# Performance work log

Hardware: AMD Instinct MI355X
Metric: run time of the kernel (lower is better)

## Reference

```python
import jax, jax.numpy as jnp
import numpy as np

N = 100000      # nodes
E = 1600000     # edges (avg degree 16)
D = 64          # in_dim == hidden_dim
L = 4           # layer_gin
G = 128         # graphs in batch
BN_EPS = 1e-5


def setup_inputs() -> dict:
    key = jax.random.key(0)
    ks = jax.random.split(key, 9)
    x = jax.random.normal(ks[0], (N, D), dtype=jnp.float32)
    edge_index = jax.random.randint(ks[1], (2, E), 0, N, dtype=jnp.int32)
    batch = jnp.sort(jax.random.randint(ks[2], (N,), 0, G, dtype=jnp.int32))
    s = 0.05
    W1 = jax.random.normal(ks[3], (L, D, D), dtype=jnp.float32) * s
    b1 = jax.random.normal(ks[4], (L, D), dtype=jnp.float32) * s
    gamma = jnp.ones((L, D), dtype=jnp.float32)
    beta = jnp.zeros((L, D), dtype=jnp.float32)
    W2 = jax.random.normal(ks[5], (L, D, D), dtype=jnp.float32) * s
    b2 = jax.random.normal(ks[6], (L, D), dtype=jnp.float32) * s
    return dict(x=x, edge_index=edge_index, batch=batch,
                W1=W1, b1=b1, gamma=gamma, beta=beta, W2=W2, b2=b2)


def reference(x, edge_index, batch, W1, b1, gamma, beta, W2, b2):
    n = x.shape[0]
    src, dst = edge_index[0], edge_index[1]  # flow source_to_target
    # in-degree for mean aggregation (clamped to avoid div-by-zero)
    deg = jax.ops.segment_sum(jnp.ones(src.shape, x.dtype), dst, num_segments=n)
    inv_deg = 1.0 / jnp.maximum(deg, 1.0)
    # graph sizes for global mean pool
    gcnt = jax.ops.segment_sum(jnp.ones((n,), x.dtype), batch, num_segments=G)
    inv_gcnt = 1.0 / jnp.maximum(gcnt, 1.0)

    h = x
    node_pool = jnp.zeros((n, W2.shape[-1]), x.dtype)
    g_pool = jnp.zeros((G, W2.shape[-1]), x.dtype)
    for l in range(L):  # small fixed layer count
        # scatter-mean neighbor aggregation: [E,D] gather -> segment_sum
        agg = jax.ops.segment_sum(h[src], dst, num_segments=n) * inv_deg[:, None]
        z = (h + agg) @ W1[l] + b1[l]          # eps=0: (1+eps)*x + mean_j x_j
        mu = z.mean(axis=0)
        var = z.var(axis=0)                     # biased, as torch BatchNorm1d
        z = (z - mu) * jax.lax.rsqrt(var + BN_EPS) * gamma[l] + beta[l]
        h = jax.nn.relu(z) @ W2[l] + b2[l]
        node_pool = node_pool + h
        g_pool = g_pool + jax.ops.segment_sum(h, batch, num_segments=G) * inv_gcnt[:, None]
    return node_pool, g_pool
```

## Files before the change

kernel.cpp:

```cpp
#include <hip/hip_runtime.h>

#define N_NODES 100000
#define N_EDGES 1600000
#define DIM 64
#define NLAYER 4
#define NGRAPH 128
#define BN_EPS 1e-5f
#define NSHARD 16
#define AGG_CHUNK 16

typedef unsigned short ushort_t;
typedef unsigned int uint_t;
typedef __attribute__((ext_vector_type(8))) short short8;
typedef __attribute__((ext_vector_type(4))) float f32x4;

__device__ __forceinline__ ushort_t f2bf(float f) {
    uint_t u = __float_as_uint(f);
    uint_t r = (u + 0x7FFFu + ((u >> 16) & 1u)) >> 16;
    return (ushort_t)r;
}
__device__ __forceinline__ float bf2f(ushort_t u) {
    return __uint_as_float((uint_t)u << 16);
}
__device__ __forceinline__ void bf8_to_f32(const uint4 v, float f[8]) {
    f[0] = __uint_as_float(v.x << 16);
    f[1] = __uint_as_float(v.x & 0xFFFF0000u);
    f[2] = __uint_as_float(v.y << 16);
    f[3] = __uint_as_float(v.y & 0xFFFF0000u);
    f[4] = __uint_as_float(v.z << 16);
    f[5] = __uint_as_float(v.z & 0xFFFF0000u);
    f[6] = __uint_as_float(v.w << 16);
    f[7] = __uint_as_float(v.w & 0xFFFF0000u);
}


__global__ void k_hist(const int* __restrict__ ei, int* __restrict__ cntS,
                       int* __restrict__ rank) {
    int e = blockIdx.x * blockDim.x + threadIdx.x;
    if (e < N_EDGES) {
        int d = ei[N_EDGES + e];
        int s = blockIdx.x & (NSHARD - 1);
        rank[e] = atomicAdd(&cntS[s * N_NODES + d], 1);
    }
}

__global__ void k_sumsh(int* __restrict__ cntS, int* __restrict__ cnt) {
    int i = blockIdx.x * blockDim.x + threadIdx.x;
    if (i < N_NODES) {
        int run = 0;
#pragma unroll
        for (int s = 0; s < NSHARD; s++) {
            int c = cntS[s * N_NODES + i];
            cntS[s * N_NODES + i] = run;
            run += c;
        }
        cnt[i] = run;
    }
}

__global__ void k_scan1(const int* __restrict__ cnt, int* __restrict__ exc,
                        int* __restrict__ bsums) {
    __shared__ int s[256];
    int i = blockIdx.x * 256 + threadIdx.x;
    int v = (i < N_NODES) ? cnt[i] : 0;
    s[threadIdx.x] = v;
    __syncthreads();
    for (int off = 1; off < 256; off <<= 1) {
        int t = (threadIdx.x >= off) ? s[threadIdx.x - off] : 0;
        __syncthreads();
        s[threadIdx.x] += t;
        __syncthreads();
    }
    if (i < N_NODES) exc[i] = s[threadIdx.x] - v;
    if (threadIdx.x == 255) bsums[blockIdx.x] = s[255];
}

__global__ void k_scan2(const int* __restrict__ bsums, int* __restrict__ boffs, int nb) {
    __shared__ int s[512];
    int v = ((int)threadIdx.x < nb) ? bsums[threadIdx.x] : 0;
    s[threadIdx.x] = v;
    __syncthreads();
    for (int off = 1; off < 512; off <<= 1) {
        int t = (threadIdx.x >= off) ? s[threadIdx.x - off] : 0;
        __syncthreads();
        s[threadIdx.x] += t;
        __syncthreads();
    }
    if ((int)threadIdx.x < nb) boffs[threadIdx.x] = s[threadIdx.x] - v;
}

__global__ void k_scan3(int* __restrict__ exc, const int* __restrict__ boffs) {
    int i = blockIdx.x * 256 + threadIdx.x;
    if (i < N_NODES) exc[i] += boffs[blockIdx.x];
}

__global__ void k_fill(const int* __restrict__ ei, const int* __restrict__ rowptr,
                       const int* __restrict__ cntS, const int* __restrict__ rank,
                       int* __restrict__ csr) {
    int e = blockIdx.x * blockDim.x + threadIdx.x;
    if (e < N_EDGES) {
        int d = ei[N_EDGES + e];
        int s = blockIdx.x & (NSHARD - 1);
        csr[rowptr[d] + cntS[s * N_NODES + d] + rank[e]] = ei[e];
    }
}

__global__ void k_prep(const int* __restrict__ cnt, const int* __restrict__ batch,
                       float* __restrict__ invdeg, float* __restrict__ invg) {
    int i = blockIdx.x * blockDim.x + threadIdx.x;
    if (i < N_NODES) invdeg[i] = 1.0f / (float)max(cnt[i], 1);
    if (i < NGRAPH) {
        int key = i, lo = 0, hi = N_NODES;
        while (lo < hi) { int m = (lo + hi) >> 1; if (batch[m] < key) lo = m + 1; else hi = m; }
        int a = lo;
        key = i + 1; lo = 0; hi = N_NODES;
        while (lo < hi) { int m = (lo + hi) >> 1; if (batch[m] < key) lo = m + 1; else hi = m; }
        invg[i] = 1.0f / (float)max(lo - a, 1);
    }
}

__global__ void k_xcast(const float* __restrict__ x, ushort_t* __restrict__ xh) {
    int i = blockIdx.x * blockDim.x + threadIdx.x;
    if (i < N_NODES * 16) {
        const float4 v = ((const float4*)x)[i];
        ushort4 u;
        u.x = f2bf(v.x); u.y = f2bf(v.y); u.z = f2bf(v.z); u.w = f2bf(v.w);
        ((ushort4*)xh)[i] = u;
    }
}

__device__ __forceinline__ void grp8b(const ushort_t* __restrict__ h,
                                      const int* __restrict__ cp,
                                      int e, int deg, int q, int r,
                                      float acc[8]) {
    const int last = deg - 1;
    const int e0 = e + q;
    int i0 = cp[min(e0, last)];
    float m0 = (e0 < deg) ? 1.f : 0.f;
    const uint4 v = *(const uint4*)(h + (size_t)i0 * 64 + r * 8);
    float f[8];
    bf8_to_f32(v, f);
#pragma unroll
    for (int j = 0; j < 8; j++) acc[j] = fmaf(f[j], m0, acc[j]);
}


__global__ __launch_bounds__(256, 4)
void k_passA(const ushort_t* __restrict__ h, const float* __restrict__ W1,
             const float* __restrict__ b1,
             const int* __restrict__ rowptr, const int* __restrict__ cnt,
             const int* __restrict__ csr, const float* __restrict__ invdeg,
             float* __restrict__ z, float* __restrict__ colsum,
             float* __restrict__ colsumsq) {
    __shared__ ushort_t wfrag[512 * 8];
    __shared__ uint_t smt[4][16 * 36];
    __shared__ float red[128];

    const int w = threadIdx.x >> 6;
    const int lane = threadIdx.x & 63;
    const int q = lane >> 3;
    const int r = lane & 7;
    const int wid = __builtin_amdgcn_readfirstlane((blockIdx.x << 2) | w);
    const bool active = wid < (N_NODES / AGG_CHUNK);
    const int n0 = (active ? wid : 0) * AGG_CHUNK;

    for (int s = threadIdx.x; s < 512; s += 256) {
        const int hh = s >> 8, c = (s >> 6) & 3, L = s & 63;
        const int kb = hh * 32 + ((L >> 4) * 8);
        const int out = c * 16 + (L & 15);
        uint_t* dst = (uint_t*)&wfrag[s * 8];
#pragma unroll
        for (int j2 = 0; j2 < 4; j2++) {
            const float lo = W1[(kb + 2 * j2) * 64 + out];
            const float hi = W1[(kb + 2 * j2 + 1) * 64 + out];
            dst[j2] = (uint_t)f2bf(lo) | ((uint_t)f2bf(hi) << 16);
        }
    }
    if (threadIdx.x < 128) red[threadIdx.x] = 0.f;
    __syncthreads();

    if (active) {
        for (int pp = 0; pp < AGG_CHUNK; pp += 2) {
            const int n = n0 + pp;
            const int sa = rowptr[n],     da = cnt[n];
            const int sb = rowptr[n + 1], db = cnt[n + 1];
            const float idga = invdeg[n], idgb = invdeg[n + 1];
            const int* __restrict__ ca = csr + sa;
            const int* __restrict__ cb = csr + sb;

            float aa[8] = {0,0,0,0,0,0,0,0};
            float ab[8] = {0,0,0,0,0,0,0,0};
            const int mm = min(da, db);
            int e = 0;
            for (; e < mm; e += 8) {
                grp8b(h, ca, e, da, q, r, aa);
                grp8b(h, cb, e, db, q, r, ab);
            }
            for (; e < da; e += 8) grp8b(h, ca, e, da, q, r, aa);
            for (; e < db; e += 8) grp8b(h, cb, e, db, q, r, ab);

#pragma unroll
            for (int j = 0; j < 8; j++) {
                aa[j] += __shfl_xor(aa[j], 8, 64);
                aa[j] += __shfl_xor(aa[j], 16, 64);
                aa[j] += __shfl_xor(aa[j], 32, 64);
                ab[j] += __shfl_xor(ab[j], 8, 64);
                ab[j] += __shfl_xor(ab[j], 16, 64);
                ab[j] += __shfl_xor(ab[j], 32, 64);
            }

            const uint4 sva = *(const uint4*)(h + (size_t)n * 64 + r * 8);
            const uint4 svb = *(const uint4*)(h + (size_t)(n + 1) * 64 + r * 8);
            float sa8[8], sb8[8];
            bf8_to_f32(sva, sa8);
            bf8_to_f32(svb, sb8);
            float ta[8], tb[8];
#pragma unroll
            for (int j = 0; j < 8; j++) {
                ta[j] = fmaf(aa[j], idga, sa8[j]);
                tb[j] = fmaf(ab[j], idgb, sb8[j]);
            }

            if (q < 2) {
                const int row = pp + q;
                uint_t* dst = &smt[w][row * 36 + r * 4];
#pragma unroll
                for (int j2 = 0; j2 < 4; j2++) {
                    const float lo = q ? tb[2 * j2]     : ta[2 * j2];
                    const float hi = q ? tb[2 * j2 + 1] : ta[2 * j2 + 1];
                    dst[j2] = (uint_t)f2bf(lo) | ((uint_t)f2bf(hi) << 16);
                }
            }
        }
    }
    __syncthreads();

    const int m = lane & 15;
    const int quad = lane >> 4;
    const short8 a0 = *(const short8*)&smt[w][m * 36 + quad * 4];
    const short8 a1 = *(const short8*)&smt[w][m * 36 + 16 + quad * 4];

    float lsum[4], lsq[4];
#pragma unroll
    for (int c = 0; c < 4; c++) {
        const short8 b0 = *(const short8*)&wfrag[(size_t)(c * 64 + lane) * 8];
        const short8 b1f = *(const short8*)&wfrag[(size_t)((4 + c) * 64 + lane) * 8];
        f32x4 D = {0.f, 0.f, 0.f, 0.f};
        D = __builtin_amdgcn_mfma_f32_16x16x32_bf16(a0, b0, D, 0, 0, 0);
        D = __builtin_amdgcn_mfma_f32_16x16x32_bf16(a1, b1f, D, 0, 0, 0);
        const float bv = b1[c * 16 + m];
        float s = 0.f, sq = 0.f;
#pragma unroll
        for (int reg = 0; reg < 4; reg++) {
            const float zv = D[reg] + bv;
            if (active) {
                const int node = n0 + quad * 4 + reg;
                __builtin_nontemporal_store(zv, &z[(size_t)node * 64 + c * 16 + m]);
            }
            s += zv;
            sq += zv * zv;
        }
        lsum[c] = s;
        lsq[c] = sq;
    }

    if (active) {
#pragma unroll
        for (int c = 0; c < 4; c++) {
            float s = lsum[c], sq = lsq[c];
            s += __shfl_xor(s, 16, 64);
            s += __shfl_xor(s, 32, 64);
            sq += __shfl_xor(sq, 16, 64);
            sq += __shfl_xor(sq, 32, 64);
            if (quad == 0) {
                atomicAdd(&red[c * 16 + m], s);
                atomicAdd(&red[64 + c * 16 + m], sq);
            }
        }
    }
    __syncthreads();
    if (threadIdx.x < 64) {
        atomicAdd(&colsum[threadIdx.x], red[threadIdx.x]);
        atomicAdd(&colsumsq[threadIdx.x], red[64 + threadIdx.x]);
    }
}


__global__ __launch_bounds__(256, 4)
void k_passB(const float* __restrict__ z, const float* __restrict__ W2,
             const float* __restrict__ b2, const float* __restrict__ colsum,
             const float* __restrict__ colsumsq, const float* __restrict__ gamma,
             const float* __restrict__ beta, ushort_t* __restrict__ hout) {
    __shared__ ushort_t wfrag[512 * 8];
    __shared__ float sscale[64], sshift[64];
    __shared__ float ltile[4][16 * 68];

    const int w = threadIdx.x >> 6;
    const int lane = threadIdx.x & 63;
    const int wid = __builtin_amdgcn_readfirstlane((blockIdx.x << 2) | w);
    const bool active = wid < (N_NODES / 16);
    const int n0 = (active ? wid : 0) * 16;

    for (int s = threadIdx.x; s < 512; s += 256) {
        const int hh = s >> 8, c = (s >> 6) & 3, L = s & 63;
        const int kb = hh * 32 + ((L >> 4) * 8);
        const int out = c * 16 + (L & 15);
        uint_t* dst = (uint_t*)&wfrag[s * 8];
#pragma unroll
        for (int j2 = 0; j2 < 4; j2++) {
            const float lo = W2[(kb + 2 * j2) * 64 + out];
            const float hi = W2[(kb + 2 * j2 + 1) * 64 + out];
            dst[j2] = (uint_t)f2bf(lo) | ((uint_t)f2bf(hi) << 16);
        }
    }
    if (threadIdx.x < 64) {
        const float invn = 1.0f / (float)N_NODES;
        const float mu = colsum[threadIdx.x] * invn;
        const float var = colsumsq[threadIdx.x] * invn - mu * mu;
        const float sc = gamma[threadIdx.x] * rsqrtf(var + BN_EPS);
        sscale[threadIdx.x] = sc;
        sshift[threadIdx.x] = beta[threadIdx.x] - mu * sc;
    }
    __syncthreads();

    const int m = lane & 15;
    const int quad = lane >> 4;

    const float* zp = z + (size_t)(n0 + m) * 64;
    const f32x4 za = __builtin_nontemporal_load((const f32x4*)(zp + quad * 8));
    const f32x4 zb = __builtin_nontemporal_load((const f32x4*)(zp + quad * 8 + 4));
    const f32x4 zc = __builtin_nontemporal_load((const f32x4*)(zp + 32 + quad * 8));
    const f32x4 zd = __builtin_nontemporal_load((const f32x4*)(zp + 32 + quad * 8 + 4));
    const f32x4 c0 = *(const f32x4*)&sscale[quad * 8];
    const f32x4 c1 = *(const f32x4*)&sscale[quad * 8 + 4];
    const f32x4 c2 = *(const f32x4*)&sscale[32 + quad * 8];
    const f32x4 c3 = *(const f32x4*)&sscale[32 + quad * 8 + 4];
    const f32x4 h0 = *(const f32x4*)&sshift[quad * 8];
    const f32x4 h1v = *(const f32x4*)&sshift[quad * 8 + 4];
    const f32x4 h2v = *(const f32x4*)&sshift[32 + quad * 8];
    const f32x4 h3v = *(const f32x4*)&sshift[32 + quad * 8 + 4];

    float r0[8], r1[8];
#pragma unroll
    for (int j = 0; j < 4; j++) {
        r0[j]     = fmaxf(fmaf(za[j], c0[j], h0[j]), 0.f);
        r0[4 + j] = fmaxf(fmaf(zb[j], c1[j], h1v[j]), 0.f);
        r1[j]     = fmaxf(fmaf(zc[j], c2[j], h2v[j]), 0.f);
        r1[4 + j] = fmaxf(fmaf(zd[j], c3[j], h3v[j]), 0.f);
    }
    union { uint_t u[4]; short8 v; } pa0, pa1;
#pragma unroll
    for (int j2 = 0; j2 < 4; j2++) {
        pa0.u[j2] = (uint_t)f2bf(r0[2 * j2]) | ((uint_t)f2bf(r0[2 * j2 + 1]) << 16);
        pa1.u[j2] = (uint_t)f2bf(r1[2 * j2]) | ((uint_t)f2bf(r1[2 * j2 + 1]) << 16);
    }
    const short8 a0 = pa0.v;
    const short8 a1 = pa1.v;

#pragma unroll
    for (int c = 0; c < 4; c++) {
        const short8 b0 = *(const short8*)&wfrag[(size_t)(c * 64 + lane) * 8];
        const short8 b1f = *(const short8*)&wfrag[(size_t)((4 + c) * 64 + lane) * 8];
        f32x4 D = {0.f, 0.f, 0.f, 0.f};
        D = __builtin_amdgcn_mfma_f32_16x16x32_bf16(a0, b0, D, 0, 0, 0);
        D = __builtin_amdgcn_mfma_f32_16x16x32_bf16(a1, b1f, D, 0, 0, 0);
        const float bv = b2[c * 16 + m];
#pragma unroll
        for (int reg = 0; reg < 4; reg++)
            ltile[w][(quad * 4 + reg) * 68 + c * 16 + m] = D[reg] + bv;
    }

    if (active) {
#pragma unroll
        for (int n = 0; n < 16; n++) {
            const float hv = ltile[w][n * 68 + lane];
            hout[(size_t)(n0 + n) * 64 + lane] = f2bf(hv);
        }
    }
}


#define POOL_CHUNK 64

__global__ void k_pool(const ushort_t* __restrict__ h1, const ushort_t* __restrict__ h2,
                       const ushort_t* __restrict__ h3, const ushort_t* __restrict__ h4,
                       const int* __restrict__ batch, float* __restrict__ node_pool,
                       float* __restrict__ gacc) {
    const int lane = threadIdx.x & 63;
    const int wid = (blockIdx.x << 2) | (threadIdx.x >> 6);
    const int n0 = wid * POOL_CHUNK;
    if (n0 >= N_NODES) return;
    const int n1 = min(N_NODES, n0 + POOL_CHUNK);
    int curg = -1;
    float ga = 0.f;
    for (int n = n0; n < n1; n++) {
        const size_t off = (size_t)n * 64 + lane;
        const float v = bf2f(h1[off]) + bf2f(h2[off]) + bf2f(h3[off]) + bf2f(h4[off]);
        __builtin_nontemporal_store(v, &node_pool[off]);
        const int g = batch[n];
        if (g != curg) {
            if (curg >= 0) atomicAdd(&gacc[curg * 64 + lane], ga);
            ga = 0.f;
            curg = g;
        }
        ga += v;
    }
    if (curg >= 0) atomicAdd(&gacc[curg * 64 + lane], ga);
}

__global__ void k_gfinal(const float* __restrict__ gacc, const float* __restrict__ invg,
                         float* __restrict__ gout) {
    int i = blockIdx.x * blockDim.x + threadIdx.x;
    if (i < NGRAPH * 64) gout[i] = gacc[i] * invg[i >> 6];
}


extern "C" void kernel_launch(void* const* d_in, const int* in_sizes, int n_in,
                              void* d_out, int out_size, void* d_ws, size_t ws_size,
                              hipStream_t stream) {
    (void)in_sizes; (void)n_in; (void)out_size; (void)ws_size;
    const float* x     = (const float*)d_in[0];
    const int*   ei    = (const int*)d_in[1];
    const int*   batch = (const int*)d_in[2];
    const float* W1    = (const float*)d_in[3];
    const float* b1    = (const float*)d_in[4];
    const float* gamma = (const float*)d_in[5];
    const float* beta  = (const float*)d_in[6];
    const float* W2    = (const float*)d_in[7];
    const float* b2    = (const float*)d_in[8];
    float* out = (float*)d_out;

    size_t o = 0;
    size_t o_cntS    = o; o += (size_t)NSHARD * N_NODES;
    size_t o_colsum  = o; o += (size_t)NLAYER * 64;
    size_t o_colsq   = o; o += (size_t)NLAYER * 64;
    size_t o_gacc    = o; o += (size_t)NGRAPH * 64;
    size_t zero_elems = o;
    size_t o_cnt     = o; o += N_NODES;
    size_t o_rowptr  = o; o += N_NODES;
    size_t o_bsums   = o; o += 512;
    size_t o_boffs   = o; o += 512;
    size_t o_invdeg  = o; o += N_NODES;
    size_t o_invg    = o; o += NGRAPH;
    size_t o_rank    = o; o += N_EDGES;
    size_t o_csr     = o; o += N_EDGES;
    size_t o_bufA    = o; o += (size_t)N_NODES * 64;
    size_t o_h1      = o; o += (size_t)N_NODES * 32;
    size_t o_h2      = o; o += (size_t)N_NODES * 32;
    size_t o_h3      = o; o += (size_t)N_NODES * 32;
    size_t o_xh      = o; o += (size_t)N_NODES * 32;

    int*   wsi = (int*)d_ws;
    float* wsf = (float*)d_ws;
    int*      cntS   = wsi + o_cntS;
    float*    colsum = wsf + o_colsum;
    float*    colsq  = wsf + o_colsq;
    float*    gacc   = wsf + o_gacc;
    int*      cnt    = wsi + o_cnt;
    int*      rowptr = wsi + o_rowptr;
    int*      bsums  = wsi + o_bsums;
    int*      boffs  = wsi + o_boffs;
    float*    invdeg = wsf + o_invdeg;
    float*    invg   = wsf + o_invg;
    int*      rank   = wsi + o_rank;
    int*      csr    = wsi + o_csr;
    float*    bufA   = wsf + o_bufA;
    ushort_t* hb0    = (ushort_t*)(wsi + o_h1);
    ushort_t* hb1    = (ushort_t*)(wsi + o_h2);
    ushort_t* hb2    = (ushort_t*)(wsi + o_h3);
    ushort_t* xh     = (ushort_t*)(wsi + o_xh);

    hipMemsetAsync(d_ws, 0, zero_elems * 4, stream);

    const int eb = (N_EDGES + 255) / 256;
    const int nb = (N_NODES + 255) / 256;

    k_hist<<<eb, 256, 0, stream>>>(ei, cntS, rank);
    k_xcast<<<(N_NODES * 16 + 255) / 256, 256, 0, stream>>>(x, xh);
    k_sumsh<<<nb, 256, 0, stream>>>(cntS, cnt);
    k_scan1<<<nb, 256, 0, stream>>>(cnt, rowptr, bsums);
    k_scan2<<<1, 512, 0, stream>>>(bsums, boffs, nb);
    k_scan3<<<nb, 256, 0, stream>>>(rowptr, boffs);
    k_prep<<<nb, 256, 0, stream>>>(cnt, batch, invdeg, invg);
    k_fill<<<eb, 256, 0, stream>>>(ei, rowptr, cntS, rank, csr);

    const ushort_t* hin[NLAYER]  = {xh,  hb0, hb1, hb2};
    ushort_t*       hoz[NLAYER]  = {hb0, hb1, hb2, xh};

    const int gridA = (N_NODES / AGG_CHUNK + 3) / 4;
    for (int l = 0; l < NLAYER; l++) {
        k_passA<<<gridA, 256, 0, stream>>>(hin[l], W1 + l * 4096, b1 + l * 64,
                                           rowptr, cnt, csr, invdeg,
                                           bufA, colsum + l * 64, colsq + l * 64);
        k_passB<<<gridA, 256, 0, stream>>>(bufA, W2 + l * 4096, b2 + l * 64,
                                           colsum + l * 64, colsq + l * 64,
                                           gamma + l * 64, beta + l * 64, hoz[l]);
    }
    const int gridP = (N_NODES + POOL_CHUNK * 4 - 1) / (POOL_CHUNK * 4);
    k_pool<<<gridP, 256, 0, stream>>>(hb0, hb1, hb2, xh, batch, out, gacc);
    k_gfinal<<<32, 256, 0, stream>>>(gacc, invg, out + (size_t)N_NODES * 64);
}
```

Before: 571.7 us.

## Split feature gather into quarter-column passes with quartered bf16 layout

Stores node features in a column-quartered bf16 layout (4 slabs of 16 columns), so each aggregation pass gathers only a 3.2 MB slab that can stay cache-resident. Aggregation is split into a separate k_gq kernel launched four times per layer, and the GEMM reads its input from global memory. The CSR build drops the sharded histogram in favour of a single atomic counter per node and pads rows to multiples of 4. The cost is extra launches, an extra write and read of the aggregated tensor, a second layout write in passB, and more atomic contention in the histogram.

```diff
diff --git a/kernel.cpp b/kernel.cpp
--- a/kernel.cpp
+++ b/kernel.cpp
@@ -6,11 +6,12 @@
 #define NLAYER 4
 #define NGRAPH 128
 #define BN_EPS 1e-5f
-#define NSHARD 16
 #define AGG_CHUNK 16
+#define NCHUNK (N_NODES / AGG_CHUNK)
 
 typedef unsigned short ushort_t;
 typedef unsigned int uint_t;
+typedef unsigned long long ull_t;
 typedef __attribute__((ext_vector_type(8))) short short8;
 typedef __attribute__((ext_vector_type(4))) float f32x4;
 
@@ -22,39 +23,20 @@
 __device__ __forceinline__ float bf2f(ushort_t u) {
     return __uint_as_float((uint_t)u << 16);
 }
-__device__ __forceinline__ void bf8_to_f32(const uint4 v, float f[8]) {
+__device__ __forceinline__ void bf4_to_f32(const uint2 v, float f[4]) {
     f[0] = __uint_as_float(v.x << 16);
     f[1] = __uint_as_float(v.x & 0xFFFF0000u);
     f[2] = __uint_as_float(v.y << 16);
     f[3] = __uint_as_float(v.y & 0xFFFF0000u);
-    f[4] = __uint_as_float(v.z << 16);
-    f[5] = __uint_as_float(v.z & 0xFFFF0000u);
-    f[6] = __uint_as_float(v.w << 16);
-    f[7] = __uint_as_float(v.w & 0xFFFF0000u);
-}
-
-
-__global__ void k_hist(const int* __restrict__ ei, int* __restrict__ cntS,
+}
+
+
+__global__ void k_hist(const int* __restrict__ ei, int* __restrict__ cnt,
                        int* __restrict__ rank) {
     int e = blockIdx.x * blockDim.x + threadIdx.x;
     if (e < N_EDGES) {
         int d = ei[N_EDGES + e];
-        int s = blockIdx.x & (NSHARD - 1);
-        rank[e] = atomicAdd(&cntS[s * N_NODES + d], 1);
-    }
-}
-
-__global__ void k_sumsh(int* __restrict__ cntS, int* __restrict__ cnt) {
-    int i = blockIdx.x * blockDim.x + threadIdx.x;
-    if (i < N_NODES) {
-        int run = 0;
-#pragma unroll
-        for (int s = 0; s < NSHARD; s++) {
-            int c = cntS[s * N_NODES + i];
-            cntS[s * N_NODES + i] = run;
-            run += c;
-        }
-        cnt[i] = run;
+        rank[e] = atomicAdd(&cnt[d], 1);
     }
 }
 
@@ -62,7 +44,7 @@
                         int* __restrict__ bsums) {
     __shared__ int s[256];
     int i = blockIdx.x * 256 + threadIdx.x;
-    int v = (i < N_NODES) ? cnt[i] : 0;
+    int v = (i < N_NODES) ? ((cnt[i] + 3) & ~3) : 0;
     s[threadIdx.x] = v;
     __syncthreads();
     for (int off = 1; off < 256; off <<= 1) {
@@ -94,14 +76,12 @@
     if (i < N_NODES) exc[i] += boffs[blockIdx.x];
 }
 
-__global__ void k_fill(const int* __restrict__ ei, const int* __restrict__ rowptr,
-                       const int* __restrict__ cntS, const int* __restrict__ rank,
-                       int* __restrict__ csr) {
+__global__ void k_fill(const int* __restrict__ ei, const int* __restrict__ rowptr4,
+                       const int* __restrict__ rank, int* __restrict__ csr) {
     int e = blockIdx.x * blockDim.x + threadIdx.x;
     if (e < N_EDGES) {
         int d = ei[N_EDGES + e];
-        int s = blockIdx.x & (NSHARD - 1);
-        csr[rowptr[d] + cntS[s * N_NODES + d] + rank[e]] = ei[e];
+        csr[rowptr4[d] + rank[e]] = ei[e];
     }
 }
 
@@ -119,49 +99,90 @@
     }
 }
 
-__global__ void k_xcast(const float* __restrict__ x, ushort_t* __restrict__ xh) {
+__global__ void k_xcastq(const float* __restrict__ x, ushort_t* __restrict__ xq) {
     int i = blockIdx.x * blockDim.x + threadIdx.x;
-    if (i < N_NODES * 16) {
-        const float4 v = ((const float4*)x)[i];
-        ushort4 u;
-        u.x = f2bf(v.x); u.y = f2bf(v.y); u.z = f2bf(v.z); u.w = f2bf(v.w);
-        ((ushort4*)xh)[i] = u;
-    }
-}
-
-__device__ __forceinline__ void grp8b(const ushort_t* __restrict__ h,
-                                      const int* __restrict__ cp,
-                                      int e, int deg, int q, int r,
-                                      float acc[8]) {
-    const int last = deg - 1;
-    const int e0 = e + q;
-    int i0 = cp[min(e0, last)];
-    float m0 = (e0 < deg) ? 1.f : 0.f;
-    const uint4 v = *(const uint4*)(h + (size_t)i0 * 64 + r * 8);
-    float f[8];
-    bf8_to_f32(v, f);
-#pragma unroll
-    for (int j = 0; j < 8; j++) acc[j] = fmaf(f[j], m0, acc[j]);
+    if (i < N_NODES * 32) {
+        const int n = i >> 5, p = i & 31;
+        const float lo = x[(size_t)n * 64 + 2 * p];
+        const float hi = x[(size_t)n * 64 + 2 * p + 1];
+        const uint_t d = (uint_t)f2bf(lo) | ((uint_t)f2bf(hi) << 16);
+        const int q = p >> 3, ci = p & 7;
+        ((uint_t*)xq)[((size_t)q * N_NODES + n) * 8 + ci] = d;
+    }
+}
+
+
+__global__ __launch_bounds__(256, 8)
+void k_gq(const ushort_t* __restrict__ hq, const int* __restrict__ rowptr4,
+          const int* __restrict__ cnt, const int* __restrict__ csr,
+          const float* __restrict__ invdeg, ushort_t* __restrict__ tq, int qtr) {
+    const int lane = threadIdx.x & 63;
+    const int s = lane >> 2;
+    const int c4 = lane & 3;
+    const int wid = (blockIdx.x << 2) | (threadIdx.x >> 6);
+    if (wid >= NCHUNK) return;
+    const int n = wid * AGG_CHUNK + s;
+
+    const size_t qoff = (size_t)qtr * N_NODES * 16;
+    const ushort_t* __restrict__ hs = hq + qoff;
+    ushort_t* __restrict__ ts = (ushort_t*)tq + qoff;
+
+    const int* __restrict__ cp = csr + rowptr4[n];
+    const int deg = cnt[n];
+    int dmax = deg;
+    dmax = max(dmax, __shfl_xor(dmax, 4, 64));
+    dmax = max(dmax, __shfl_xor(dmax, 8, 64));
+    dmax = max(dmax, __shfl_xor(dmax, 16, 64));
+    dmax = max(dmax, __shfl_xor(dmax, 32, 64));
+
+    float acc[4] = {0.f, 0.f, 0.f, 0.f};
+    for (int e = 0; e < dmax; e += 4) {
+        const int i0 = __builtin_nontemporal_load(&cp[e]);
+        const int i1 = __builtin_nontemporal_load(&cp[e + 1]);
+        const int i2 = __builtin_nontemporal_load(&cp[e + 2]);
+        const int i3 = __builtin_nontemporal_load(&cp[e + 3]);
+        const int ia[4] = {i0, i1, i2, i3};
+#pragma unroll
+        for (int k = 0; k < 4; k++) {
+            if (e + k < deg) {
+                const uint2 v = *(const uint2*)(hs + (size_t)(uint_t)ia[k] * 16 + (c4 << 2));
+                float f[4];
+                bf4_to_f32(v, f);
+                acc[0] += f[0];
+                acc[1] += f[1];
+                acc[2] += f[2];
+                acc[3] += f[3];
+            }
+        }
+    }
+
+    const float idg = invdeg[n];
+    const uint2 sv = *(const uint2*)(hs + (size_t)n * 16 + (c4 << 2));
+    float sf[4];
+    bf4_to_f32(sv, sf);
+    const float t0 = fmaf(acc[0], idg, sf[0]);
+    const float t1 = fmaf(acc[1], idg, sf[1]);
+    const float t2 = fmaf(acc[2], idg, sf[2]);
+    const float t3 = fmaf(acc[3], idg, sf[3]);
+    const uint_t d0 = (uint_t)f2bf(t0) | ((uint_t)f2bf(t1) << 16);
+    const uint_t d1 = (uint_t)f2bf(t2) | ((uint_t)f2bf(t3) << 16);
+    uint_t* dst = (uint_t*)(ts + (size_t)n * 16) + (c4 << 1);
+    __builtin_nontemporal_store(d0, dst);
+    __builtin_nontemporal_store(d1, dst + 1);
 }
 
 
 __global__ __launch_bounds__(256, 4)
-void k_passA(const ushort_t* __restrict__ h, const float* __restrict__ W1,
-             const float* __restrict__ b1,
-             const int* __restrict__ rowptr, const int* __restrict__ cnt,
-             const int* __restrict__ csr, const float* __restrict__ invdeg,
-             float* __restrict__ z, float* __restrict__ colsum,
-             float* __restrict__ colsumsq) {
+void k_mmA(const ushort_t* __restrict__ t, const float* __restrict__ W1,
+           const float* __restrict__ b1, float* __restrict__ z,
+           float* __restrict__ colsum, float* __restrict__ colsumsq) {
     __shared__ ushort_t wfrag[512 * 8];
-    __shared__ uint_t smt[4][16 * 36];
     __shared__ float red[128];
 
     const int w = threadIdx.x >> 6;
     const int lane = threadIdx.x & 63;
-    const int q = lane >> 3;
-    const int r = lane & 7;
     const int wid = __builtin_amdgcn_readfirstlane((blockIdx.x << 2) | w);
-    const bool active = wid < (N_NODES / AGG_CHUNK);
+    const bool active = wid < NCHUNK;
     const int n0 = (active ? wid : 0) * AGG_CHUNK;
 
     for (int s = threadIdx.x; s < 512; s += 256) {
@@ -179,66 +200,13 @@
     if (threadIdx.x < 128) red[threadIdx.x] = 0.f;
     __syncthreads();
 
-    if (active) {
-        for (int pp = 0; pp < AGG_CHUNK; pp += 2) {
-            const int n = n0 + pp;
-            const int sa = rowptr[n],     da = cnt[n];
-            const int sb = rowptr[n + 1], db = cnt[n + 1];
-            const float idga = invdeg[n], idgb = invdeg[n + 1];
-            const int* __restrict__ ca = csr + sa;
-            const int* __restrict__ cb = csr + sb;
-
-            float aa[8] = {0,0,0,0,0,0,0,0};
-            float ab[8] = {0,0,0,0,0,0,0,0};
-            const int mm = min(da, db);
-            int e = 0;
-            for (; e < mm; e += 8) {
-                grp8b(h, ca, e, da, q, r, aa);
-                grp8b(h, cb, e, db, q, r, ab);
-            }
-            for (; e < da; e += 8) grp8b(h, ca, e, da, q, r, aa);
-            for (; e < db; e += 8) grp8b(h, cb, e, db, q, r, ab);
-
-#pragma unroll
-            for (int j = 0; j < 8; j++) {
-                aa[j] += __shfl_xor(aa[j], 8, 64);
-                aa[j] += __shfl_xor(aa[j], 16, 64);
-                aa[j] += __shfl_xor(aa[j], 32, 64);
-                ab[j] += __shfl_xor(ab[j], 8, 64);
-                ab[j] += __shfl_xor(ab[j], 16, 64);
-                ab[j] += __shfl_xor(ab[j], 32, 64);
-            }
-
-            const uint4 sva = *(const uint4*)(h + (size_t)n * 64 + r * 8);
-            const uint4 svb = *(const uint4*)(h + (size_t)(n + 1) * 64 + r * 8);
-            float sa8[8], sb8[8];
-            bf8_to_f32(sva, sa8);
-            bf8_to_f32(svb, sb8);
-            float ta[8], tb[8];
-#pragma unroll
-            for (int j = 0; j < 8; j++) {
-                ta[j] = fmaf(aa[j], idga, sa8[j]);
-                tb[j] = fmaf(ab[j], idgb, sb8[j]);
-            }
-
-            if (q < 2) {
-                const int row = pp + q;
-                uint_t* dst = &smt[w][row * 36 + r * 4];
-#pragma unroll
-                for (int j2 = 0; j2 < 4; j2++) {
-                    const float lo = q ? tb[2 * j2]     : ta[2 * j2];
-                    const float hi = q ? tb[2 * j2 + 1] : ta[2 * j2 + 1];
-                    dst[j2] = (uint_t)f2bf(lo) | ((uint_t)f2bf(hi) << 16);
-                }
-            }
-        }
-    }
-    __syncthreads();
-
     const int m = lane & 15;
     const int quad = lane >> 4;
-    const short8 a0 = *(const short8*)&smt[w][m * 36 + quad * 4];
-    const short8 a1 = *(const short8*)&smt[w][m * 36 + 16 + quad * 4];
+    const int node = n0 + m;
+    const short8 a0 = *(const short8*)(t +
+        ((size_t)((quad >> 1) * N_NODES) + node) * 16 + ((quad & 1) << 3));
+    const short8 a1 = *(const short8*)(t +
+        ((size_t)(((quad >> 1) + 2) * N_NODES) + node) * 16 + ((quad & 1) << 3));
 
     float lsum[4], lsq[4];
 #pragma unroll
@@ -254,8 +222,8 @@
         for (int reg = 0; reg < 4; reg++) {
             const float zv = D[reg] + bv;
             if (active) {
-                const int node = n0 + quad * 4 + reg;
-                __builtin_nontemporal_store(zv, &z[(size_t)node * 64 + c * 16 + m]);
+                const int nd = n0 + quad * 4 + reg;
+                __builtin_nontemporal_store(zv, &z[(size_t)nd * 64 + c * 16 + m]);
             }
             s += zv;
             sq += zv * zv;
@@ -290,7 +258,8 @@
 void k_passB(const float* __restrict__ z, const float* __restrict__ W2,
              const float* __restrict__ b2, const float* __restrict__ colsum,
              const float* __restrict__ colsumsq, const float* __restrict__ gamma,
-             const float* __restrict__ beta, ushort_t* __restrict__ hout) {
+             const float* __restrict__ beta, ushort_t* __restrict__ hout,
+             ushort_t* __restrict__ houtq) {
     __shared__ ushort_t wfrag[512 * 8];
     __shared__ float sscale[64], sshift[64];
     __shared__ float ltile[4][16 * 68];
@@ -298,8 +267,8 @@
     const int w = threadIdx.x >> 6;
     const int lane = threadIdx.x & 63;
     const int wid = __builtin_amdgcn_readfirstlane((blockIdx.x << 2) | w);
-    const bool active = wid < (N_NODES / 16);
-    const int n0 = (active ? wid : 0) * 16;
+    const bool active = wid < NCHUNK;
+    const int n0 = (active ? wid : 0) * AGG_CHUNK;
 
     for (int s = threadIdx.x; s < 512; s += 256) {
         const int hh = s >> 8, c = (s >> 6) & 3, L = s & 63;
@@ -371,10 +340,14 @@
     }
 
     if (active) {
+        const int qs = lane >> 4, ci = lane & 15;
 #pragma unroll
         for (int n = 0; n < 16; n++) {
             const float hv = ltile[w][n * 68 + lane];
-            hout[(size_t)(n0 + n) * 64 + lane] = f2bf(hv);
+            const ushort_t b = f2bf(hv);
+            hout[(size_t)(n0 + n) * 64 + lane] = b;
+            if (houtq)
+                houtq[((size_t)qs * N_NODES + (n0 + n)) * 16 + ci] = b;
         }
     }
 }
@@ -431,32 +404,33 @@
     float* out = (float*)d_out;
 
     size_t o = 0;
-    size_t o_cntS    = o; o += (size_t)NSHARD * N_NODES;
+    size_t o_cnt     = o; o += N_NODES;
     size_t o_colsum  = o; o += (size_t)NLAYER * 64;
     size_t o_colsq   = o; o += (size_t)NLAYER * 64;
     size_t o_gacc    = o; o += (size_t)NGRAPH * 64;
     size_t zero_elems = o;
-    size_t o_cnt     = o; o += N_NODES;
     size_t o_rowptr  = o; o += N_NODES;
     size_t o_bsums   = o; o += 512;
     size_t o_boffs   = o; o += 512;
     size_t o_invdeg  = o; o += N_NODES;
     size_t o_invg    = o; o += NGRAPH;
     size_t o_rank    = o; o += N_EDGES;
-    size_t o_csr     = o; o += N_EDGES;
-    size_t o_bufA    = o; o += (size_t)N_NODES * 64;
+    size_t o_csr     = o; o += N_EDGES + 3 * N_NODES + 64;
+    size_t o_z       = o; o += (size_t)N_NODES * 64;
+    size_t o_t       = o; o += (size_t)N_NODES * 32;
+    size_t o_sA      = o; o += (size_t)N_NODES * 32;
+    size_t o_sB      = o; o += (size_t)N_NODES * 32;
+    size_t o_h0      = o; o += (size_t)N_NODES * 32;
     size_t o_h1      = o; o += (size_t)N_NODES * 32;
     size_t o_h2      = o; o += (size_t)N_NODES * 32;
     size_t o_h3      = o; o += (size_t)N_NODES * 32;
-    size_t o_xh      = o; o += (size_t)N_NODES * 32;
 
     int*   wsi = (int*)d_ws;
     float* wsf = (float*)d_ws;
-    int*      cntS   = wsi + o_cntS;
+    int*      cnt    = wsi + o_cnt;
     float*    colsum = wsf + o_colsum;
     float*    colsq  = wsf + o_colsq;
     float*    gacc   = wsf + o_gacc;
-    int*      cnt    = wsi + o_cnt;
     int*      rowptr = wsi + o_rowptr;
     int*      bsums  = wsi + o_bsums;
     int*      boffs  = wsi + o_boffs;
@@ -464,39 +438,42 @@
     float*    invg   = wsf + o_invg;
     int*      rank   = wsi + o_rank;
     int*      csr    = wsi + o_csr;
-    float*    bufA   = wsf + o_bufA;
-    ushort_t* hb0    = (ushort_t*)(wsi + o_h1);
-    ushort_t* hb1    = (ushort_t*)(wsi + o_h2);
-    ushort_t* hb2    = (ushort_t*)(wsi + o_h3);
-    ushort_t* xh     = (ushort_t*)(wsi + o_xh);
+    float*    zbuf   = wsf + o_z;
+    ushort_t* tbuf   = (ushort_t*)(wsi + o_t);
+    ushort_t* sA     = (ushort_t*)(wsi + o_sA);
+    ushort_t* sB     = (ushort_t*)(wsi + o_sB);
+    ushort_t* hrm[NLAYER] = {(ushort_t*)(wsi + o_h0), (ushort_t*)(wsi + o_h1),
+                             (ushort_t*)(wsi + o_h2), (ushort_t*)(wsi + o_h3)};
 
     hipMemsetAsync(d_ws, 0, zero_elems * 4, stream);
 
     const int eb = (N_EDGES + 255) / 256;
     const int nb = (N_NODES + 255) / 256;
 
-    k_hist<<<eb, 256, 0, stream>>>(ei, cntS, rank);
-    k_xcast<<<(N_NODES * 16 + 255) / 256, 256, 0, stream>>>(x, xh);
-    k_sumsh<<<nb, 256, 0, stream>>>(cntS, cnt);
+    k_hist<<<eb, 256, 0, stream>>>(ei, cnt, rank);
+    k_xcastq<<<(N_NODES * 32 + 255) / 256, 256, 0, stream>>>(x, sA);
     k_scan1<<<nb, 256, 0, stream>>>(cnt, rowptr, bsums);
     k_scan2<<<1, 512, 0, stream>>>(bsums, boffs, nb);
     k_scan3<<<nb, 256, 0, stream>>>(rowptr, boffs);
     k_prep<<<nb, 256, 0, stream>>>(cnt, batch, invdeg, invg);
-    k_fill<<<eb, 256, 0, stream>>>(ei, rowptr, cntS, rank, csr);
-
-    const ushort_t* hin[NLAYER]  = {xh,  hb0, hb1, hb2};
-    ushort_t*       hoz[NLAYER]  = {hb0, hb1, hb2, xh};
-
-    const int gridA = (N_NODES / AGG_CHUNK + 3) / 4;
+    k_fill<<<eb, 256, 0, stream>>>(ei, rowptr, rank, csr);
+
+    const int gridC = (NCHUNK + 3) / 4;
+    const ushort_t* sin[NLAYER] = {sA, sB, sA, sB};
+    ushort_t*       sout[NLAYER] = {sB, sA, sB, nullptr};
     for (int l = 0; l < NLAYER; l++) {
-        k_passA<<<gridA, 256, 0, stream>>>(hin[l], W1 + l * 4096, b1 + l * 64,
-                                           rowptr, cnt, csr, invdeg,
-                                           bufA, colsum + l * 64, colsq + l * 64);
-        k_passB<<<gridA, 256, 0, stream>>>(bufA, W2 + l * 4096, b2 + l * 64,
+        for (int qq = 0; qq < 4; qq++)
+            k_gq<<<gridC, 256, 0, stream>>>(sin[l], rowptr, cnt, csr, invdeg,
+                                            tbuf, qq);
+        k_mmA<<<gridC, 256, 0, stream>>>(tbuf, W1 + l * 4096, b1 + l * 64,
+                                         zbuf, colsum + l * 64, colsq + l * 64);
+        k_passB<<<gridC, 256, 0, stream>>>(zbuf, W2 + l * 4096, b2 + l * 64,
                                            colsum + l * 64, colsq + l * 64,
-                                           gamma + l * 64, beta + l * 64, hoz[l]);
+                                           gamma + l * 64, beta + l * 64,
+                                           hrm[l], sout[l]);
     }
     const int gridP = (N_NODES + POOL_CHUNK * 4 - 1) / (POOL_CHUNK * 4);
-    k_pool<<<gridP, 256, 0, stream>>>(hb0, hb1, hb2, xh, batch, out, gacc);
+    k_pool<<<gridP, 256, 0, stream>>>(hrm[0], hrm[1], hrm[2], hrm[3],
+                                      batch, out, gacc);
     k_gfinal<<<32, 256, 0, stream>>>(gacc, invg, out + (size_t)N_NODES * 64);
 }
```

New measurement: 792.2 us. 1.39x slower.

## Store bf16 aggregated input instead of fp32 z; recompute W1 GEMM in passB

Applied to the files above, without the earlier changes.

passA now writes the bf16 pre-GEMM tile (h+agg) to global memory in place of the fp32 z output, and still computes column statistics for BatchNorm. passB reloads that half-size bf16 tile, recomputes the first GEMM with MFMA, applies BN+ReLU through shared memory, then runs the second GEMM. The intermediate round trip shrinks from fp32 64-wide to bf16 64-wide per node, at the cost of a redundant MFMA pass and extra LDS for W1 fragments. A separate prep kernel is also merged into k_scan3 to remove one launch.

```diff
diff --git a/kernel.cpp b/kernel.cpp
--- a/kernel.cpp
+++ b/kernel.cpp
@@ -8,11 +8,13 @@
 #define BN_EPS 1e-5f
 #define NSHARD 16
 #define AGG_CHUNK 16
+#define NCHUNK (N_NODES / AGG_CHUNK)
 
 typedef unsigned short ushort_t;
 typedef unsigned int uint_t;
 typedef __attribute__((ext_vector_type(8))) short short8;
 typedef __attribute__((ext_vector_type(4))) float f32x4;
+typedef __attribute__((ext_vector_type(4))) uint_t uintx4;
 
 __device__ __forceinline__ ushort_t f2bf(float f) {
     uint_t u = __float_as_uint(f);
@@ -89,9 +91,22 @@
     if ((int)threadIdx.x < nb) boffs[threadIdx.x] = s[threadIdx.x] - v;
 }
 
-__global__ void k_scan3(int* __restrict__ exc, const int* __restrict__ boffs) {
+__global__ void k_scan3(int* __restrict__ exc, const int* __restrict__ boffs,
+                        const int* __restrict__ cnt, const int* __restrict__ batch,
+                        float* __restrict__ invdeg, float* __restrict__ invg) {
     int i = blockIdx.x * 256 + threadIdx.x;
-    if (i < N_NODES) exc[i] += boffs[blockIdx.x];
+    if (i < N_NODES) {
+        exc[i] += boffs[blockIdx.x];
+        invdeg[i] = 1.0f / (float)max(cnt[i], 1);
+    }
+    if (i < NGRAPH) {
+        int key = i, lo = 0, hi = N_NODES;
+        while (lo < hi) { int m = (lo + hi) >> 1; if (batch[m] < key) lo = m + 1; else hi = m; }
+        int a = lo;
+        key = i + 1; lo = 0; hi = N_NODES;
+        while (lo < hi) { int m = (lo + hi) >> 1; if (batch[m] < key) lo = m + 1; else hi = m; }
+        invg[i] = 1.0f / (float)max(lo - a, 1);
+    }
 }
 
 __global__ void k_fill(const int* __restrict__ ei, const int* __restrict__ rowptr,
@@ -102,20 +117,6 @@
         int d = ei[N_EDGES + e];
         int s = blockIdx.x & (NSHARD - 1);
         csr[rowptr[d] + cntS[s * N_NODES + d] + rank[e]] = ei[e];
-    }
-}
-
-__global__ void k_prep(const int* __restrict__ cnt, const int* __restrict__ batch,
-                       float* __restrict__ invdeg, float* __restrict__ invg) {
-    int i = blockIdx.x * blockDim.x + threadIdx.x;
-    if (i < N_NODES) invdeg[i] = 1.0f / (float)max(cnt[i], 1);
-    if (i < NGRAPH) {
-        int key = i, lo = 0, hi = N_NODES;
-        while (lo < hi) { int m = (lo + hi) >> 1; if (batch[m] < key) lo = m + 1; else hi = m; }
-        int a = lo;
-        key = i + 1; lo = 0; hi = N_NODES;
-        while (lo < hi) { int m = (lo + hi) >> 1; if (batch[m] < key) lo = m + 1; else hi = m; }
-        invg[i] = 1.0f / (float)max(lo - a, 1);
     }
 }
 
@@ -150,7 +151,7 @@
              const float* __restrict__ b1,
              const int* __restrict__ rowptr, const int* __restrict__ cnt,
              const int* __restrict__ csr, const float* __restrict__ invdeg,
-             float* __restrict__ z, float* __restrict__ colsum,
+             ushort_t* __restrict__ tglob, float* __restrict__ colsum,
              float* __restrict__ colsumsq) {
     __shared__ ushort_t wfrag[512 * 8];
     __shared__ uint_t smt[4][16 * 36];
@@ -161,7 +162,7 @@
     const int q = lane >> 3;
     const int r = lane & 7;
     const int wid = __builtin_amdgcn_readfirstlane((blockIdx.x << 2) | w);
-    const bool active = wid < (N_NODES / AGG_CHUNK);
+    const bool active = wid < NCHUNK;
     const int n0 = (active ? wid : 0) * AGG_CHUNK;
 
     for (int s = threadIdx.x; s < 512; s += 256) {
@@ -233,7 +234,17 @@
             }
         }
     }
-    __syncthreads();
+
+    if (active) {
+        const int rr = lane >> 2, c4 = lane & 3;
+        const uint_t* src = &smt[w][rr * 36 + c4 * 8];
+        uintx4 v0, v1;
+#pragma unroll
+        for (int j = 0; j < 4; j++) { v0[j] = src[j]; v1[j] = src[4 + j]; }
+        uintx4* dst = (uintx4*)((uint_t*)tglob + (size_t)(n0 + rr) * 32) + c4 * 2;
+        __builtin_nontemporal_store(v0, dst);
+        __builtin_nontemporal_store(v1, dst + 1);
+    }
 
     const int m = lane & 15;
     const int quad = lane >> 4;
@@ -253,10 +264,6 @@
 #pragma unroll
         for (int reg = 0; reg < 4; reg++) {
             const float zv = D[reg] + bv;
-            if (active) {
-                const int node = n0 + quad * 4 + reg;
-                __builtin_nontemporal_store(zv, &z[(size_t)node * 64 + c * 16 + m]);
-            }
             s += zv;
             sq += zv * zv;
         }
@@ -287,29 +294,33 @@
 
 
 __global__ __launch_bounds__(256, 4)
-void k_passB(const float* __restrict__ z, const float* __restrict__ W2,
+void k_passB(const ushort_t* __restrict__ t, const float* __restrict__ W1,
+             const float* __restrict__ b1, const float* __restrict__ W2,
              const float* __restrict__ b2, const float* __restrict__ colsum,
              const float* __restrict__ colsumsq, const float* __restrict__ gamma,
              const float* __restrict__ beta, ushort_t* __restrict__ hout) {
-    __shared__ ushort_t wfrag[512 * 8];
+    __shared__ ushort_t wf1[512 * 8];
+    __shared__ ushort_t wf2[512 * 8];
     __shared__ float sscale[64], sshift[64];
     __shared__ float ltile[4][16 * 68];
 
     const int w = threadIdx.x >> 6;
     const int lane = threadIdx.x & 63;
     const int wid = __builtin_amdgcn_readfirstlane((blockIdx.x << 2) | w);
-    const bool active = wid < (N_NODES / 16);
-    const int n0 = (active ? wid : 0) * 16;
-
-    for (int s = threadIdx.x; s < 512; s += 256) {
-        const int hh = s >> 8, c = (s >> 6) & 3, L = s & 63;
+    const bool active = wid < NCHUNK;
+    const int n0 = (active ? wid : 0) * AGG_CHUNK;
+
+    for (int s = threadIdx.x; s < 1024; s += 256) {
+        const int which = s >> 9, t2 = s & 511;
+        const int hh = t2 >> 8, c = (t2 >> 6) & 3, L = t2 & 63;
         const int kb = hh * 32 + ((L >> 4) * 8);
         const int out = c * 16 + (L & 15);
-        uint_t* dst = (uint_t*)&wfrag[s * 8];
+        const float* W = which ? W2 : W1;
+        uint_t* dst = (uint_t*)&(which ? wf2 : wf1)[t2 * 8];
 #pragma unroll
         for (int j2 = 0; j2 < 4; j2++) {
-            const float lo = W2[(kb + 2 * j2) * 64 + out];
-            const float hi = W2[(kb + 2 * j2 + 1) * 64 + out];
+            const float lo = W[(kb + 2 * j2) * 64 + out];
+            const float hi = W[(kb + 2 * j2 + 1) * 64 + out];
             dst[j2] = (uint_t)f2bf(lo) | ((uint_t)f2bf(hi) << 16);
         }
     }
@@ -326,27 +337,33 @@
     const int m = lane & 15;
     const int quad = lane >> 4;
 
-    const float* zp = z + (size_t)(n0 + m) * 64;
-    const f32x4 za = __builtin_nontemporal_load((const f32x4*)(zp + quad * 8));
-    const f32x4 zb = __builtin_nontemporal_load((const f32x4*)(zp + quad * 8 + 4));
-    const f32x4 zc = __builtin_nontemporal_load((const f32x4*)(zp + 32 + quad * 8));
-    const f32x4 zd = __builtin_nontemporal_load((const f32x4*)(zp + 32 + quad * 8 + 4));
-    const f32x4 c0 = *(const f32x4*)&sscale[quad * 8];
-    const f32x4 c1 = *(const f32x4*)&sscale[quad * 8 + 4];
-    const f32x4 c2 = *(const f32x4*)&sscale[32 + quad * 8];
-    const f32x4 c3 = *(const f32x4*)&sscale[32 + quad * 8 + 4];
-    const f32x4 h0 = *(const f32x4*)&sshift[quad * 8];
-    const f32x4 h1v = *(const f32x4*)&sshift[quad * 8 + 4];
-    const f32x4 h2v = *(const f32x4*)&sshift[32 + quad * 8];
-    const f32x4 h3v = *(const f32x4*)&sshift[32 + quad * 8 + 4];
-
+    const ushort_t* tp = t + (size_t)(n0 + m) * 64;
+    const short8 a0 = __builtin_nontemporal_load((const short8*)(tp + quad * 8));
+    const short8 a1 = __builtin_nontemporal_load((const short8*)(tp + 32 + quad * 8));
+
+#pragma unroll
+    for (int c = 0; c < 4; c++) {
+        const short8 b0 = *(const short8*)&wf1[(size_t)(c * 64 + lane) * 8];
+        const short8 b1f = *(const short8*)&wf1[(size_t)((4 + c) * 64 + lane) * 8];
+        f32x4 D = {0.f, 0.f, 0.f, 0.f};
+        D = __builtin_amdgcn_mfma_f32_16x16x32_bf16(a0, b0, D, 0, 0, 0);
+        D = __builtin_amdgcn_mfma_f32_16x16x32_bf16(a1, b1f, D, 0, 0, 0);
+        const int col = c * 16 + m;
+        const float bv = b1[col];
+        const float sc = sscale[col], sh = sshift[col];
+#pragma unroll
+        for (int reg = 0; reg < 4; reg++) {
+            const float zv = D[reg] + bv;
+            ltile[w][(quad * 4 + reg) * 68 + col] = fmaxf(fmaf(zv, sc, sh), 0.f);
+        }
+    }
+
+    const float* lr = &ltile[w][m * 68];
     float r0[8], r1[8];
 #pragma unroll
-    for (int j = 0; j < 4; j++) {
-        r0[j]     = fmaxf(fmaf(za[j], c0[j], h0[j]), 0.f);
-        r0[4 + j] = fmaxf(fmaf(zb[j], c1[j], h1v[j]), 0.f);
-        r1[j]     = fmaxf(fmaf(zc[j], c2[j], h2v[j]), 0.f);
-        r1[4 + j] = fmaxf(fmaf(zd[j], c3[j], h3v[j]), 0.f);
+    for (int j = 0; j < 8; j++) {
+        r0[j] = lr[quad * 8 + j];
+        r1[j] = lr[32 + quad * 8 + j];
     }
     union { uint_t u[4]; short8 v; } pa0, pa1;
 #pragma unroll
@@ -354,16 +371,16 @@
         pa0.u[j2] = (uint_t)f2bf(r0[2 * j2]) | ((uint_t)f2bf(r0[2 * j2 + 1]) << 16);
         pa1.u[j2] = (uint_t)f2bf(r1[2 * j2]) | ((uint_t)f2bf(r1[2 * j2 + 1]) << 16);
     }
-    const short8 a0 = pa0.v;
-    const short8 a1 = pa1.v;
+    const short8 c0 = pa0.v;
+    const short8 c1 = pa1.v;
 
 #pragma unroll
     for (int c = 0; c < 4; c++) {
-        const short8 b0 = *(const short8*)&wfrag[(size_t)(c * 64 + lane) * 8];
-        const short8 b1f = *(const short8*)&wfrag[(size_t)((4 + c) * 64 + lane) * 8];
+        const short8 b0 = *(const short8*)&wf2[(size_t)(c * 64 + lane) * 8];
+        const short8 b1f = *(const short8*)&wf2[(size_t)((4 + c) * 64 + lane) * 8];
         f32x4 D = {0.f, 0.f, 0.f, 0.f};
-        D = __builtin_amdgcn_mfma_f32_16x16x32_bf16(a0, b0, D, 0, 0, 0);
-        D = __builtin_amdgcn_mfma_f32_16x16x32_bf16(a1, b1f, D, 0, 0, 0);
+        D = __builtin_amdgcn_mfma_f32_16x16x32_bf16(c0, b0, D, 0, 0, 0);
+        D = __builtin_amdgcn_mfma_f32_16x16x32_bf16(c1, b1f, D, 0, 0, 0);
         const float bv = b2[c * 16 + m];
 #pragma unroll
         for (int reg = 0; reg < 4; reg++)
@@ -444,10 +461,10 @@
     size_t o_invg    = o; o += NGRAPH;
     size_t o_rank    = o; o += N_EDGES;
     size_t o_csr     = o; o += N_EDGES;
-    size_t o_bufA    = o; o += (size_t)N_NODES * 64;
+    size_t o_t       = o; o += (size_t)N_NODES * 32;
+    size_t o_h0      = o; o += (size_t)N_NODES * 32;
     size_t o_h1      = o; o += (size_t)N_NODES * 32;
     size_t o_h2      = o; o += (size_t)N_NODES * 32;
-    size_t o_h3      = o; o += (size_t)N_NODES * 32;
     size_t o_xh      = o; o += (size_t)N_NODES * 32;
 
     int*   wsi = (int*)d_ws;
@@ -464,10 +481,10 @@
     float*    invg   = wsf + o_invg;
     int*      rank   = wsi + o_rank;
     int*      csr    = wsi + o_csr;
-    float*    bufA   = wsf + o_bufA;
-    ushort_t* hb0    = (ushort_t*)(wsi + o_h1);
-    ushort_t* hb1    = (ushort_t*)(wsi + o_h2);
-    ushort_t* hb2    = (ushort_t*)(wsi + o_h3);
+    ushort_t* tbuf   = (ushort_t*)(wsi + o_t);
+    ushort_t* hb0    = (ushort_t*)(wsi + o_h0);
+    ushort_t* hb1    = (ushort_t*)(wsi + o_h1);
+    ushort_t* hb2    = (ushort_t*)(wsi + o_h2);
     ushort_t* xh     = (ushort_t*)(wsi + o_xh);
 
     hipMemsetAsync(d_ws, 0, zero_elems * 4, stream);
@@ -480,19 +497,19 @@
     k_sumsh<<<nb, 256, 0, stream>>>(cntS, cnt);
     k_scan1<<<nb, 256, 0, stream>>>(cnt, rowptr, bsums);
     k_scan2<<<1, 512, 0, stream>>>(bsums, boffs, nb);
-    k_scan3<<<nb, 256, 0, stream>>>(rowptr, boffs);
-    k_prep<<<nb, 256, 0, stream>>>(cnt, batch, invdeg, invg);
+    k_scan3<<<nb, 256, 0, stream>>>(rowptr, boffs, cnt, batch, invdeg, invg);
     k_fill<<<eb, 256, 0, stream>>>(ei, rowptr, cntS, rank, csr);
 
     const ushort_t* hin[NLAYER]  = {xh,  hb0, hb1, hb2};
     ushort_t*       hoz[NLAYER]  = {hb0, hb1, hb2, xh};
 
-    const int gridA = (N_NODES / AGG_CHUNK + 3) / 4;
+    const int gridA = (NCHUNK + 3) / 4;
     for (int l = 0; l < NLAYER; l++) {
         k_passA<<<gridA, 256, 0, stream>>>(hin[l], W1 + l * 4096, b1 + l * 64,
                                            rowptr, cnt, csr, invdeg,
-                                           bufA, colsum + l * 64, colsq + l * 64);
-        k_passB<<<gridA, 256, 0, stream>>>(bufA, W2 + l * 4096, b2 + l * 64,
+                                           tbuf, colsum + l * 64, colsq + l * 64);
+        k_passB<<<gridA, 256, 0, stream>>>(tbuf, W1 + l * 4096, b1 + l * 64,
+                                           W2 + l * 4096, b2 + l * 64,
                                            colsum + l * 64, colsq + l * 64,
                                            gamma + l * 64, beta + l * 64, hoz[l]);
     }
```

Measured after the change: 575.8 us. About the same (+0.7%).
